# Performance work log

Measured on AMD Instinct MI355X. Metric: run time of the kernel, lower is better.

## Reference

```python
import jax, jax.numpy as jnp
import numpy as np


def setup_inputs() -> dict:
    key = jax.random.key(0)
    k1, k2 = jax.random.split(key)
    B, C, H, W = 64, 64, 64, 64
    map1 = jax.random.normal(k1, (B, C, H, W), dtype=jnp.float32)
    map2 = jax.random.normal(k2, (B, C, H, W), dtype=jnp.float32)
    return {"map1": map1, "map2": map2}


def reference(map1, map2):
    # conv2d(map1, map2) with equal spatial dims -> [B,B,1,1]; .diag() keeps
    # only the per-sample full cross-correlation: c_i = sum(map1[i]*map2[i]).
    corr = jnp.einsum('bchw,bchw->b', map1, map2)          # [B]
    corr = corr / jnp.linalg.norm(corr)                    # L2-normalize over batch
    corr = 1.0 - corr
    # out[i] = map1[i] + map2[i] * corr[i]
    return map1 + map2 * corr[:, None, None, None]
```

## Files before the change

kernel.cpp:

```cpp
#include <hip/hip_runtime.h>


#define THREADS 256
#define BLOCKS_PER_BATCH 32
#define VEC_PER_BATCH 65536
#define VEC_PER_BLOCK 2048
#define VEC_PER_THREAD 8
#define NBATCH 64

__global__ __launch_bounds__(THREADS) void corr_reduce_kernel(
    const float4* __restrict__ m1, const float4* __restrict__ m2,
    float* __restrict__ corr) {
  const int b = blockIdx.y;
  const int base = b * VEC_PER_BATCH + blockIdx.x * VEC_PER_BLOCK + threadIdx.x;

  float acc = 0.0f;
#pragma unroll
  for (int k = 0; k < VEC_PER_THREAD; ++k) {
    const float4 a = m1[base + k * THREADS];
    const float4 c = m2[base + k * THREADS];
    acc = fmaf(a.x, c.x, acc);
    acc = fmaf(a.y, c.y, acc);
    acc = fmaf(a.z, c.z, acc);
    acc = fmaf(a.w, c.w, acc);
  }

#pragma unroll
  for (int off = 32; off > 0; off >>= 1) acc += __shfl_down(acc, off);

  if ((threadIdx.x & 63) == 0) atomicAdd(&corr[b], acc);
}

__global__ __launch_bounds__(THREADS) void corr_apply_kernel(
    const float4* __restrict__ m1, const float4* __restrict__ m2,
    const float* __restrict__ corr, float4* __restrict__ out) {
  __shared__ float c_sh;
  const int b = blockIdx.y;

  if (threadIdx.x < 64) {
    const float v = corr[threadIdx.x];
    float sq = v * v;
#pragma unroll
    for (int off = 32; off > 0; off >>= 1) sq += __shfl_down(sq, off);
    if (threadIdx.x == 0) c_sh = 1.0f - corr[b] * rsqrtf(sq);
  }
  __syncthreads();
  const float c = c_sh;

  const int base = b * VEC_PER_BATCH + blockIdx.x * VEC_PER_BLOCK + threadIdx.x;
#pragma unroll
  for (int k = 0; k < VEC_PER_THREAD; ++k) {
    const float4 a = m1[base + k * THREADS];
    const float4 v = m2[base + k * THREADS];
    float4 o;
    o.x = fmaf(v.x, c, a.x);
    o.y = fmaf(v.y, c, a.y);
    o.z = fmaf(v.z, c, a.z);
    o.w = fmaf(v.w, c, a.w);
    out[base + k * THREADS] = o;
  }
}

extern "C" void kernel_launch(void* const* d_in, const int* in_sizes, int n_in,
                              void* d_out, int out_size, void* d_ws, size_t ws_size,
                              hipStream_t stream) {
  const float4* m1 = (const float4*)d_in[0];
  const float4* m2 = (const float4*)d_in[1];
  float* corr = (float*)d_ws;
  float4* out = (float4*)d_out;

  hipMemsetAsync(corr, 0, NBATCH * sizeof(float), stream);

  dim3 grid(BLOCKS_PER_BATCH, NBATCH);
  corr_reduce_kernel<<<grid, THREADS, 0, stream>>>(m1, m2, corr);
  corr_apply_kernel<<<grid, THREADS, 0, stream>>>(m1, m2, corr, out);
}
```

Baseline: 216.2 us.

## Replace atomics and memset with per-block partials; prefetch apply loads before corr

The reduce kernel now writes one partial sum per block into a workspace array instead of doing per-wave atomicAdds, which also removes the hipMemsetAsync launch. The apply kernel sums the 32 partials per batch itself, and issues its first batch of m1/m2 loads before the shared-memory normalization step so load latency overlaps that work. Loads are restructured into explicit batches of four float4 and launch bounds request 8 blocks per CU. The cost is that every apply block re-reads all 2048 partials.

```diff
diff --git a/kernel.cpp b/kernel.cpp
--- a/kernel.cpp
+++ b/kernel.cpp
@@ -2,63 +2,115 @@
 
 
 #define THREADS 256
-#define BLOCKS_PER_BATCH 32
-#define VEC_PER_BATCH 65536
-#define VEC_PER_BLOCK 2048
-#define VEC_PER_THREAD 8
+#define BPB 32
+#define VPB 65536
+#define VPBLK 2048
 #define NBATCH 64
 
-__global__ __launch_bounds__(THREADS) void corr_reduce_kernel(
+__global__ __launch_bounds__(THREADS, 8) void corr_reduce_kernel(
     const float4* __restrict__ m1, const float4* __restrict__ m2,
-    float* __restrict__ corr) {
+    float* __restrict__ partials) {
   const int b = blockIdx.y;
-  const int base = b * VEC_PER_BATCH + blockIdx.x * VEC_PER_BLOCK + threadIdx.x;
+  const int base = b * VPB + blockIdx.x * VPBLK + threadIdx.x;
 
   float acc = 0.0f;
 #pragma unroll
-  for (int k = 0; k < VEC_PER_THREAD; ++k) {
-    const float4 a = m1[base + k * THREADS];
-    const float4 c = m2[base + k * THREADS];
-    acc = fmaf(a.x, c.x, acc);
-    acc = fmaf(a.y, c.y, acc);
-    acc = fmaf(a.z, c.z, acc);
-    acc = fmaf(a.w, c.w, acc);
+  for (int r = 0; r < 2; ++r) {
+    const int o = base + r * 4 * THREADS;
+    const float4 a0 = m1[o];
+    const float4 a1 = m1[o + THREADS];
+    const float4 a2 = m1[o + 2 * THREADS];
+    const float4 a3 = m1[o + 3 * THREADS];
+    const float4 c0 = m2[o];
+    const float4 c1 = m2[o + THREADS];
+    const float4 c2 = m2[o + 2 * THREADS];
+    const float4 c3 = m2[o + 3 * THREADS];
+    acc = fmaf(a0.x, c0.x, acc); acc = fmaf(a0.y, c0.y, acc);
+    acc = fmaf(a0.z, c0.z, acc); acc = fmaf(a0.w, c0.w, acc);
+    acc = fmaf(a1.x, c1.x, acc); acc = fmaf(a1.y, c1.y, acc);
+    acc = fmaf(a1.z, c1.z, acc); acc = fmaf(a1.w, c1.w, acc);
+    acc = fmaf(a2.x, c2.x, acc); acc = fmaf(a2.y, c2.y, acc);
+    acc = fmaf(a2.z, c2.z, acc); acc = fmaf(a2.w, c2.w, acc);
+    acc = fmaf(a3.x, c3.x, acc); acc = fmaf(a3.y, c3.y, acc);
+    acc = fmaf(a3.z, c3.z, acc); acc = fmaf(a3.w, c3.w, acc);
   }
 
 #pragma unroll
-  for (int off = 32; off > 0; off >>= 1) acc += __shfl_down(acc, off);
+  for (int off = 32; off > 0; off >>= 1) acc += __shfl_xor(acc, off);
 
-  if ((threadIdx.x & 63) == 0) atomicAdd(&corr[b], acc);
+  __shared__ float wsum[4];
+  const int wave = threadIdx.x >> 6;
+  if ((threadIdx.x & 63) == 0) wsum[wave] = acc;
+  __syncthreads();
+  if (threadIdx.x == 0)
+    partials[b * BPB + blockIdx.x] = wsum[0] + wsum[1] + wsum[2] + wsum[3];
 }
 
-__global__ __launch_bounds__(THREADS) void corr_apply_kernel(
+__global__ __launch_bounds__(THREADS, 8) void corr_apply_kernel(
     const float4* __restrict__ m1, const float4* __restrict__ m2,
-    const float* __restrict__ corr, float4* __restrict__ out) {
+    const float* __restrict__ partials, float4* __restrict__ out) {
+  const int b = blockIdx.y;
+  const int base = b * VPB + blockIdx.x * VPBLK + threadIdx.x;
+
+  const float4 a0 = m1[base];
+  const float4 a1 = m1[base + THREADS];
+  const float4 a2 = m1[base + 2 * THREADS];
+  const float4 a3 = m1[base + 3 * THREADS];
+  const float4 v0 = m2[base];
+  const float4 v1 = m2[base + THREADS];
+  const float4 v2 = m2[base + 2 * THREADS];
+  const float4 v3 = m2[base + 3 * THREADS];
+
   __shared__ float c_sh;
-  const int b = blockIdx.y;
-
   if (threadIdx.x < 64) {
-    const float v = corr[threadIdx.x];
-    float sq = v * v;
+    float s = 0.0f;
 #pragma unroll
-    for (int off = 32; off > 0; off >>= 1) sq += __shfl_down(sq, off);
-    if (threadIdx.x == 0) c_sh = 1.0f - corr[b] * rsqrtf(sq);
+    for (int i = 0; i < BPB; ++i) s += partials[threadIdx.x * BPB + i];
+    float sq = s * s;
+#pragma unroll
+    for (int off = 32; off > 0; off >>= 1) sq += __shfl_xor(sq, off);
+    const float cb = __shfl(s, b);
+    if (threadIdx.x == 0) c_sh = 1.0f - cb * rsqrtf(sq);
   }
   __syncthreads();
   const float c = c_sh;
 
-  const int base = b * VEC_PER_BATCH + blockIdx.x * VEC_PER_BLOCK + threadIdx.x;
-#pragma unroll
-  for (int k = 0; k < VEC_PER_THREAD; ++k) {
-    const float4 a = m1[base + k * THREADS];
-    const float4 v = m2[base + k * THREADS];
-    float4 o;
-    o.x = fmaf(v.x, c, a.x);
-    o.y = fmaf(v.y, c, a.y);
-    o.z = fmaf(v.z, c, a.z);
-    o.w = fmaf(v.w, c, a.w);
-    out[base + k * THREADS] = o;
-  }
+  float4 o;
+  o.x = fmaf(v0.x, c, a0.x); o.y = fmaf(v0.y, c, a0.y);
+  o.z = fmaf(v0.z, c, a0.z); o.w = fmaf(v0.w, c, a0.w);
+  out[base] = o;
+  o.x = fmaf(v1.x, c, a1.x); o.y = fmaf(v1.y, c, a1.y);
+  o.z = fmaf(v1.z, c, a1.z); o.w = fmaf(v1.w, c, a1.w);
+  out[base + THREADS] = o;
+  o.x = fmaf(v2.x, c, a2.x); o.y = fmaf(v2.y, c, a2.y);
+  o.z = fmaf(v2.z, c, a2.z); o.w = fmaf(v2.w, c, a2.w);
+  out[base + 2 * THREADS] = o;
+  o.x = fmaf(v3.x, c, a3.x); o.y = fmaf(v3.y, c, a3.y);
+  o.z = fmaf(v3.z, c, a3.z); o.w = fmaf(v3.w, c, a3.w);
+  out[base + 3 * THREADS] = o;
+
+  const int base2 = base + 4 * THREADS;
+  const float4 b0 = m1[base2];
+  const float4 b1 = m1[base2 + THREADS];
+  const float4 b2 = m1[base2 + 2 * THREADS];
+  const float4 b3 = m1[base2 + 3 * THREADS];
+  const float4 w0 = m2[base2];
+  const float4 w1 = m2[base2 + THREADS];
+  const float4 w2 = m2[base2 + 2 * THREADS];
+  const float4 w3 = m2[base2 + 3 * THREADS];
+
+  o.x = fmaf(w0.x, c, b0.x); o.y = fmaf(w0.y, c, b0.y);
+  o.z = fmaf(w0.z, c, b0.z); o.w = fmaf(w0.w, c, b0.w);
+  out[base2] = o;
+  o.x = fmaf(w1.x, c, b1.x); o.y = fmaf(w1.y, c, b1.y);
+  o.z = fmaf(w1.z, c, b1.z); o.w = fmaf(w1.w, c, b1.w);
+  out[base2 + THREADS] = o;
+  o.x = fmaf(w2.x, c, b2.x); o.y = fmaf(w2.y, c, b2.y);
+  o.z = fmaf(w2.z, c, b2.z); o.w = fmaf(w2.w, c, b2.w);
+  out[base2 + 2 * THREADS] = o;
+  o.x = fmaf(w3.x, c, b3.x); o.y = fmaf(w3.y, c, b3.y);
+  o.z = fmaf(w3.z, c, b3.z); o.w = fmaf(w3.w, c, b3.w);
+  out[base2 + 3 * THREADS] = o;
 }
 
 extern "C" void kernel_launch(void* const* d_in, const int* in_sizes, int n_in,
@@ -66,12 +118,10 @@
                               hipStream_t stream) {
   const float4* m1 = (const float4*)d_in[0];
   const float4* m2 = (const float4*)d_in[1];
-  float* corr = (float*)d_ws;
+  float* partials = (float*)d_ws;
   float4* out = (float4*)d_out;
 
-  hipMemsetAsync(corr, 0, NBATCH * sizeof(float), stream);
-
-  dim3 grid(BLOCKS_PER_BATCH, NBATCH);
-  corr_reduce_kernel<<<grid, THREADS, 0, stream>>>(m1, m2, corr);
-  corr_apply_kernel<<<grid, THREADS, 0, stream>>>(m1, m2, corr, out);
+  dim3 grid(BPB, NBATCH);
+  corr_reduce_kernel<<<grid, THREADS, 0, stream>>>(m1, m2, partials);
+  corr_apply_kernel<<<grid, THREADS, 0, stream>>>(m1, m2, partials, out);
 }
```

Result: faster. 186.5 us (-13.7%).

## Replace atomics and memset with per-block partials reduced inside apply kernel

Applied to the files above, without the earlier changes.

The reduce kernel now writes one partial sum per block into a 64x64 workspace instead of atomically adding into a zeroed corr array, which removes the memset launch and the atomic traffic. The apply kernel issues its m1/m2 loads first, then every block re-reduces all 4096 partials to get the norm and its batch coefficient, overlapping that small reduction with the in-flight loads. Blocks are halved in size (1024 float4 per block, 64 blocks per batch), with occupancy hints and sched barriers to batch loads. Each apply block re-reads the 16KB partials array, which adds redundant traffic.

```diff
diff --git a/kernel.cpp b/kernel.cpp
--- a/kernel.cpp
+++ b/kernel.cpp
@@ -2,61 +2,88 @@
 
 
 #define THREADS 256
-#define BLOCKS_PER_BATCH 32
-#define VEC_PER_BATCH 65536
-#define VEC_PER_BLOCK 2048
-#define VEC_PER_THREAD 8
 #define NBATCH 64
+#define BPB 64
+#define V4B 65536
+#define V4BLK 1024
 
-__global__ __launch_bounds__(THREADS) void corr_reduce_kernel(
+__global__ __launch_bounds__(THREADS, 8) void corr_reduce_kernel(
     const float4* __restrict__ m1, const float4* __restrict__ m2,
-    float* __restrict__ corr) {
+    float* __restrict__ partials) {
   const int b = blockIdx.y;
-  const int base = b * VEC_PER_BATCH + blockIdx.x * VEC_PER_BLOCK + threadIdx.x;
+  const int base = b * V4B + blockIdx.x * V4BLK + threadIdx.x;
 
-  float acc = 0.0f;
+  float4 a[4], v[4];
 #pragma unroll
-  for (int k = 0; k < VEC_PER_THREAD; ++k) {
-    const float4 a = m1[base + k * THREADS];
-    const float4 c = m2[base + k * THREADS];
-    acc = fmaf(a.x, c.x, acc);
-    acc = fmaf(a.y, c.y, acc);
-    acc = fmaf(a.z, c.z, acc);
-    acc = fmaf(a.w, c.w, acc);
+  for (int k = 0; k < 4; ++k) a[k] = m1[base + k * THREADS];
+#pragma unroll
+  for (int k = 0; k < 4; ++k) v[k] = m2[base + k * THREADS];
+  __builtin_amdgcn_sched_barrier(0);
+
+  float acc0 = 0.f, acc1 = 0.f, acc2 = 0.f, acc3 = 0.f;
+#pragma unroll
+  for (int k = 0; k < 4; ++k) {
+    acc0 = fmaf(a[k].x, v[k].x, acc0);
+    acc1 = fmaf(a[k].y, v[k].y, acc1);
+    acc2 = fmaf(a[k].z, v[k].z, acc2);
+    acc3 = fmaf(a[k].w, v[k].w, acc3);
   }
+  float acc = (acc0 + acc1) + (acc2 + acc3);
 
 #pragma unroll
-  for (int off = 32; off > 0; off >>= 1) acc += __shfl_down(acc, off);
+  for (int off = 32; off > 0; off >>= 1) acc += __shfl_xor(acc, off);
 
-  if ((threadIdx.x & 63) == 0) atomicAdd(&corr[b], acc);
+  __shared__ float wsum[4];
+  if ((threadIdx.x & 63) == 0) wsum[threadIdx.x >> 6] = acc;
+  __syncthreads();
+  if (threadIdx.x == 0)
+    partials[b * BPB + blockIdx.x] = (wsum[0] + wsum[1]) + (wsum[2] + wsum[3]);
 }
 
-__global__ __launch_bounds__(THREADS) void corr_apply_kernel(
+__global__ __launch_bounds__(THREADS, 4) void corr_apply_kernel(
     const float4* __restrict__ m1, const float4* __restrict__ m2,
-    const float* __restrict__ corr, float4* __restrict__ out) {
+    const float4* __restrict__ partials4, float4* __restrict__ out) {
+  const int b = blockIdx.y;
+  const int base = b * V4B + blockIdx.x * V4BLK + threadIdx.x;
+
+  float4 a[4], v[4];
+#pragma unroll
+  for (int k = 0; k < 4; ++k) a[k] = m1[base + k * THREADS];
+#pragma unroll
+  for (int k = 0; k < 4; ++k) v[k] = m2[base + k * THREADS];
+
+  float4 p[4];
+#pragma unroll
+  for (int k = 0; k < 4; ++k) p[k] = partials4[threadIdx.x * 4 + k];
+  __builtin_amdgcn_sched_barrier(0);
+
+  float s = 0.f;
+#pragma unroll
+  for (int k = 0; k < 4; ++k) s += (p[k].x + p[k].y) + (p[k].z + p[k].w);
+  s += __shfl_xor(s, 1);
+  s += __shfl_xor(s, 2);
+
+  __shared__ float csh[NBATCH];
   __shared__ float c_sh;
-  const int b = blockIdx.y;
-
+  if ((threadIdx.x & 3) == 0) csh[threadIdx.x >> 2] = s;
+  __syncthreads();
   if (threadIdx.x < 64) {
-    const float v = corr[threadIdx.x];
-    float sq = v * v;
+    float cv = csh[threadIdx.x];
+    float sq = cv * cv;
 #pragma unroll
-    for (int off = 32; off > 0; off >>= 1) sq += __shfl_down(sq, off);
-    if (threadIdx.x == 0) c_sh = 1.0f - corr[b] * rsqrtf(sq);
+    for (int off = 32; off > 0; off >>= 1) sq += __shfl_xor(sq, off);
+    if (threadIdx.x == 0) c_sh = 1.0f - csh[b] * rsqrtf(sq);
   }
   __syncthreads();
   const float c = c_sh;
 
-  const int base = b * VEC_PER_BATCH + blockIdx.x * VEC_PER_BLOCK + threadIdx.x;
 #pragma unroll
-  for (int k = 0; k < VEC_PER_THREAD; ++k) {
-    const float4 a = m1[base + k * THREADS];
-    const float4 v = m2[base + k * THREADS];
+  for (int k = 0; k < 4; ++k) {
     float4 o;
-    o.x = fmaf(v.x, c, a.x);
-    o.y = fmaf(v.y, c, a.y);
-    o.z = fmaf(v.z, c, a.z);
-    o.w = fmaf(v.w, c, a.w);
+    o.x = fmaf(v[k].x, c, a[k].x);
+    o.y = fmaf(v[k].y, c, a[k].y);
+    o.z = fmaf(v[k].z, c, a[k].z);
+    o.w = fmaf(v[k].w, c, a[k].w);
     out[base + k * THREADS] = o;
   }
 }
@@ -66,12 +93,10 @@
                               hipStream_t stream) {
   const float4* m1 = (const float4*)d_in[0];
   const float4* m2 = (const float4*)d_in[1];
-  float* corr = (float*)d_ws;
+  float* partials = (float*)d_ws;
   float4* out = (float4*)d_out;
 
-  hipMemsetAsync(corr, 0, NBATCH * sizeof(float), stream);
-
-  dim3 grid(BLOCKS_PER_BATCH, NBATCH);
-  corr_reduce_kernel<<<grid, THREADS, 0, stream>>>(m1, m2, corr);
-  corr_apply_kernel<<<grid, THREADS, 0, stream>>>(m1, m2, corr, out);
+  dim3 grid(BPB, NBATCH);
+  corr_reduce_kernel<<<grid, THREADS, 0, stream>>>(m1, m2, partials);
+  corr_apply_kernel<<<grid, THREADS, 0, stream>>>(m1, m2, (const float4*)partials, out);
 }
```

Result: faster. 184.0 us (-14.9%).
